# Kernel tuning notes

Measured on AMD Instinct MI355X. Metric: run time of the kernel, lower is better.

Reference implementation:

```python
import jax, jax.numpy as jnp
import numpy as np
from jax import lax

B, C, H, W = 4, 256, 64, 64
R1, R2 = 4, 8


def conv1x1(x, w, b):
    # x: [B,C,H,W], w: [O,C], b: [O]
    return jnp.einsum('bchw,oc->bohw', x, w) + b[None, :, None, None]


def dwconv3x3(x, w, b):
    # depthwise 3x3, SAME padding. w: [C,1,3,3]
    y = lax.conv_general_dilated(x, w, window_strides=(1, 1), padding='SAME',
                                 dimension_numbers=('NCHW', 'OIHW', 'NCHW'),
                                 feature_group_count=x.shape[1])
    return y + b[None, :, None, None]


def setup_inputs() -> dict:
    key = jax.random.key(0)
    ks = jax.random.split(key, 20)
    s = 0.02
    inp = {
        'x':   jax.random.normal(ks[0], (B, C, H, W), jnp.float32),
        'Wq':  jax.random.normal(ks[1], (C, C), jnp.float32) * s,
        'bq':  jnp.zeros((C,), jnp.float32),
        'Wk':  jax.random.normal(ks[2], (C, 1, 3, 3), jnp.float32) * s,
        'bk':  jnp.zeros((C,), jnp.float32),
        'Wv':  jax.random.normal(ks[3], (C, 1, 3, 3), jnp.float32) * s,
        'bv':  jnp.zeros((C,), jnp.float32),
        'Wl':  jax.random.normal(ks[4], (C, 1, 3, 3), jnp.float32) * s,
        'bl':  jnp.zeros((C,), jnp.float32),
        'Ws1': jax.random.normal(ks[5], (C // R1, C), jnp.float32) * s,
        'bs1': jnp.zeros((C // R1,), jnp.float32),
        'Ws2': jax.random.normal(ks[6], (C, C // R1), jnp.float32) * s,
        'bs2': jnp.zeros((C,), jnp.float32),
        'Wc1': jax.random.normal(ks[7], (C // R2, C), jnp.float32) * s,
        'bc1': jnp.zeros((C // R2,), jnp.float32),
        'Wc2': jax.random.normal(ks[8], (C, C // R2), jnp.float32) * s,
        'bc2': jnp.zeros((C,), jnp.float32),
        'Wo':  jax.random.normal(ks[9], (C, C), jnp.float32) * s,
        'bo':  jnp.zeros((C,), jnp.float32),
    }
    return inp


def reference(x, Wq, bq, Wk, bk, Wv, bv, Wl, bl, Ws1, bs1, Ws2, bs2,
              Wc1, bc1, Wc2, bc2, Wo, bo):
    b_, c_, h_, w_ = x.shape
    hw = h_ * w_
    scale = jnp.sqrt(jnp.float32(c_))

    q = conv1x1(x, Wq, bq).reshape(b_, c_, hw).transpose(0, 2, 1)   # [B,HW,C]
    k = dwconv3x3(x, Wk, bk).reshape(b_, c_, hw)                    # [B,C,HW]
    v_img = dwconv3x3(x, Wv, bv)                                    # [B,C,H,W]
    v = v_img.reshape(b_, c_, hw).transpose(0, 2, 1)                # [B,HW,C]

    attn = jax.nn.softmax(jnp.einsum('bnc,bcm->bnm', q, k) / scale, axis=-1)
    global_out = jnp.einsum('bnm,bmc->bnc', attn, v)                # [B,HW,C]
    global_out = global_out.transpose(0, 2, 1).reshape(b_, c_, h_, w_)

    local_out = dwconv3x3(v_img, Wl, bl)                            # [B,C,H,W]

    spatial_weight = jax.nn.sigmoid(
        conv1x1(jax.nn.relu(conv1x1(local_out, Ws1, bs1)), Ws2, bs2))

    gap = jnp.mean(global_out, axis=(2, 3), keepdims=True)          # [B,C,1,1]
    channel_weight = jax.nn.sigmoid(
        conv1x1(jax.nn.relu(conv1x1(gap, Wc1, bc1)), Wc2, bc2))     # [B,C,1,1]

    fused = global_out * channel_weight + local_out * spatial_weight
    return conv1x1(fused, Wo, bo) + x
```

## Files before the change

### kernel.cpp

```cpp
#include <hip/hip_runtime.h>
#include <hip/hip_fp8.h>
#include <stdint.h>

typedef unsigned short u16;
typedef unsigned char u8;
typedef __attribute__((ext_vector_type(8))) __bf16 bf16x8;
typedef __attribute__((ext_vector_type(8))) short short8s;
typedef __attribute__((ext_vector_type(4))) float float4v;
typedef __attribute__((ext_vector_type(16))) float floatx16;
typedef __attribute__((ext_vector_type(4))) int int4v;
typedef __attribute__((ext_vector_type(8))) int int8v;

static constexpr int NB = 4, NC = 256, NH = 64, NW = 64, NHW = 4096;
static constexpr int BC = 64;
static constexpr int NKV = 4;
static constexpr int KVCHUNK = NHW / NKV;

static constexpr size_t MB = 1ull << 20;
static constexpr size_t OFF_KBF    = 0;
static constexpr size_t OFF_LBF    = 8 * MB;
static constexpr size_t OFF_GT     = 0;
static constexpr size_t OFF_XT     = 16 * MB;
static constexpr size_t OFF_LPART  = 16 * MB;
static constexpr size_t OFF_QT8    = 24 * MB;
static constexpr size_t OFF_KT8    = 32 * MB;
static constexpr size_t OFF_V8     = 40 * MB;
static constexpr size_t OFF_LT     = 48 * MB;
static constexpr size_t OFF_OPART  = 56 * MB;
static constexpr size_t OFF_HIDT   = 88 * MB;
static constexpr size_t OFF_GAP    = OFF_HIDT + 2 * MB;
static constexpr size_t OFF_WQB    = OFF_GAP + 8 * 1024;
static constexpr size_t OFF_WS1B   = OFF_WQB + 131072;
static constexpr size_t OFF_WS2B   = OFF_WS1B + 32768;
static constexpr size_t OFF_WOB    = OFF_WS2B + 32768;

__device__ __forceinline__ float b2f(u16 h) {
    union { float f; unsigned u; } v; v.u = ((unsigned)h) << 16; return v.f;
}
__device__ __forceinline__ u16 f2b(float f) {
    union { float f; unsigned u; } v; v.f = f;
    unsigned r = v.u + 0x7fffu + ((v.u >> 16) & 1u);
    return (u16)(r >> 16);
}
__device__ __forceinline__ u8 f2f8(float f) {
    __hip_fp8_e4m3 h(f);
    return *reinterpret_cast<u8*>(&h);
}

__device__ __forceinline__ void load_lds16(const void* gsrc, void* ldst) {
    __builtin_amdgcn_global_load_lds(
        (__attribute__((address_space(1))) void*)(uintptr_t)gsrc,
        (__attribute__((address_space(3))) void*)ldst,
        16, 0, 0);
}

__global__ __launch_bounds__(256) void prep(
    const float* __restrict__ x,
    const float* __restrict__ Wq, const float* __restrict__ Ws1,
    const float* __restrict__ Ws2, const float* __restrict__ Wo,
    const float* __restrict__ Wk, const float* __restrict__ bk,
    const float* __restrict__ Wv, const float* __restrict__ bv,
    const float* __restrict__ Wl, const float* __restrict__ bl,
    u16* __restrict__ Wqb, u16* __restrict__ Ws1b, u16* __restrict__ Ws2b, u16* __restrict__ Wob,
    float* __restrict__ gap,
    u16* __restrict__ k_bf, u8* __restrict__ vN8, u16* __restrict__ local_bf,
    u16* __restrict__ xT)
{
    __shared__ __align__(16) unsigned char pshm[9216];
    const int bid = blockIdx.x;
    const int t = threadIdx.x;

    if (bid < 644) {
        int id = bid * 256 + t;
        if (id < 65536)        Wqb[id] = f2b(Wq[id]);
        else if (id < 81920)   Ws1b[id - 65536] = f2b(Ws1[id - 65536]);
        else if (id < 98304)   Ws2b[id - 81920] = f2b(Ws2[id - 81920]);
        else if (id < 163840)  Wob[id - 98304] = f2b(Wo[id - 98304]);
        else if (id < 164864)  gap[id - 163840] = 0.f;
        return;
    }
    if (bid < 2692) {
        int l = bid - 644;
        int xx0 = t & 63, cl = t >> 6;
        int y0 = (l & 7) * 8;
        int c  = ((l >> 3) & 63) * 4 + cl;
        int b  = l >> 9;
        const float* xb = x + ((size_t)b * NC + c) * NHW;
        float wk[9], wv[9], wl[9];
#pragma unroll
        for (int i = 0; i < 9; i++) { wk[i] = Wk[c*9+i]; wv[i] = Wv[c*9+i]; wl[i] = Wl[c*9+i]; }
        float bkc = bk[c], bvc = bv[c], blc = bl[c];

        auto ldx = [&](int y) -> float {
            return ((unsigned)y <= 63u) ? xb[y * 64 + xx0] : 0.f;
        };
        auto conv3 = [&](const float* w9, float a, float bm, float cc) -> float {
            float au = __shfl_up(a, 1, 64),   ad = __shfl_down(a, 1, 64);
            float bu = __shfl_up(bm, 1, 64),  bd = __shfl_down(bm, 1, 64);
            float cu = __shfl_up(cc, 1, 64),  cd = __shfl_down(cc, 1, 64);
            float al = (xx0 == 0) ? 0.f : au, ar = (xx0 == 63) ? 0.f : ad;
            float bl_ = (xx0 == 0) ? 0.f : bu, br = (xx0 == 63) ? 0.f : bd;
            float cle = (xx0 == 0) ? 0.f : cu, cr = (xx0 == 63) ? 0.f : cd;
            return w9[0]*al + w9[1]*a  + w9[2]*ar
                 + w9[3]*bl_ + w9[4]*bm + w9[5]*br
                 + w9[6]*cle + w9[7]*cc + w9[8]*cr;
        };

        float xm2 = ldx(y0 - 2), xm1 = ldx(y0 - 1), x0v = ldx(y0), xp1 = ldx(y0 + 1);
        float vm1 = (y0 - 1 >= 0) ? (bvc + conv3(wv, xm2, xm1, x0v)) : 0.f;
        float v0  = bvc + conv3(wv, xm1, x0v, xp1);

        size_t base = ((size_t)b * NC + c) * NHW;
#pragma unroll
        for (int yi = 0; yi < 8; yi++) {
            int y = y0 + yi;
            float xp2 = ldx(y + 2);
            float vp1 = (y + 1 <= 63) ? (bvc + conv3(wv, x0v, xp1, xp2)) : 0.f;
            float kk  = bkc + conv3(wk, xm1, x0v, xp1);
            float ll  = blc + conv3(wl, vm1, v0, vp1);
            size_t o = base + y * 64 + xx0;
            k_bf[o]     = f2b(kk);
            vN8[o]      = f2f8(v0);
            local_bf[o] = f2b(ll);
            xm1 = x0v; x0v = xp1; xp1 = xp2;
            vm1 = v0;  v0 = vp1;
        }
        return;
    }
    {
        u16 (*tile)[72] = reinterpret_cast<u16 (*)[72]>(pshm);
        int l = bid - 2692;
        int n0 = (l & 63) * 64;
        int c0 = ((l >> 6) & 3) * 64;
        int b  = l >> 8;
        const float* src = x + (size_t)b * NC * NHW;
        u16* dst = xT + (size_t)b * NHW * NC;
        int c = t >> 2, nb = (t & 3) * 16;
#pragma unroll
        for (int q = 0; q < 4; q++) {
            float4 v = *(const float4*)(src + (size_t)(c0 + c) * NHW + n0 + nb + q * 4);
            tile[c][nb + q * 4 + 0] = f2b(v.x);
            tile[c][nb + q * 4 + 1] = f2b(v.y);
            tile[c][nb + q * 4 + 2] = f2b(v.z);
            tile[c][nb + q * 4 + 3] = f2b(v.w);
        }
        __syncthreads();
        int cl = t & 63, ng = t >> 6;
#pragma unroll
        for (int j = 0; j < 16; j++) {
            int n = ng * 16 + j;
            dst[(size_t)(n0 + n) * NC + c0 + cl] = tile[cl][n];
        }
    }
}

__global__ __launch_bounds__(256) void mid(
    const u16* __restrict__ k_bf, const u16* __restrict__ local_bf,
    u8* __restrict__ kT8, u16* __restrict__ localT,
    const u16* __restrict__ xT, const u16* __restrict__ Wqb, const float* __restrict__ bq,
    u8* __restrict__ qT8)
{
    __shared__ __align__(16) u16 tile[64][72];
    const int t = threadIdx.x;
    const int bid = blockIdx.x;
    if (bid < 2048) {
        int n0 = (bid & 63) * 64, c0 = ((bid >> 6) & 3) * 64;
        int zb = bid >> 8, b = zb >> 1;
        const u16* src = (zb & 1) ? local_bf : k_bf;
        src += (size_t)b * NC * NHW;
        int c = t >> 2, nb = (t & 3) * 16;
        *(short8s*)&tile[c][nb]     = *(const short8s*)(src + (size_t)(c0 + c) * NHW + n0 + nb);
        *(short8s*)&tile[c][nb + 8] = *(const short8s*)(src + (size_t)(c0 + c) * NHW + n0 + nb + 8);
        __syncthreads();
        int cl = t & 63, ng = t >> 6;
        if (zb & 1) {
            u16* dst = localT + (size_t)b * NHW * NC;
#pragma unroll
            for (int j = 0; j < 16; j++) {
                int n = ng * 16 + j;
                dst[(size_t)(n0 + n) * NC + c0 + cl] = tile[cl][n];
            }
        } else {
            u8* dst = kT8 + (size_t)b * NHW * NC;
#pragma unroll
            for (int j = 0; j < 16; j++) {
                int n = ng * 16 + j;
                dst[(size_t)(n0 + n) * NC + c0 + cl] = f2f8(b2f(tile[cl][n]));
            }
        }
        return;
    }
    {
        const int w = t >> 6, lane = t & 63;
        const int lm = lane & 15, quad = lane >> 4;
        const int l = bid - 2048;
        const int b = l >> 7;
        const int s_base = (l & 127) * 32 + (w & 1) * 16;
        const int ch = (w >> 1) * 128;
        const u16* xTb = xT + (size_t)b * NHW * NC;
        u8* qTb = qT8 + (size_t)b * NHW * NC;
        bf16x8 aq[8];
#pragma unroll
        for (int kt = 0; kt < 8; kt++)
            aq[kt] = *(const bf16x8*)(xTb + (size_t)(s_base + lm) * NC + kt * 32 + quad * 8);
        float4v acc[8];
#pragma unroll
        for (int j = 0; j < 8; j++) acc[j] = (float4v){0.f, 0.f, 0.f, 0.f};
#pragma unroll
        for (int kt = 0; kt < 8; kt++) {
#pragma unroll
            for (int j = 0; j < 8; j++) {
                bf16x8 bw = *(const bf16x8*)(Wqb + (size_t)(ch + j * 16 + lm) * 256 + kt * 32 + quad * 8);
                acc[j] = __builtin_amdgcn_mfma_f32_16x16x32_bf16(aq[kt], bw, acc[j], 0, 0, 0);
            }
        }
#pragma unroll
        for (int j = 0; j < 8; j++) {
            int cout = ch + j * 16 + lm;
            float bb = bq[cout];
#pragma unroll
            for (int r = 0; r < 4; r++) {
                int s = s_base + quad * 4 + r;
                qTb[(size_t)s * NC + cout] = f2f8(acc[j][r] + bb);
            }
        }
    }
}

__device__ __forceinline__ void stage_tiles(
    const u8* __restrict__ kb, const u8* __restrict__ vb8, int kv0,
    u8* KlB, u8* VlB, int w, int lane)
{
#pragma unroll
    for (int i = 0; i < 4; i++) {
        int g = (w * 4 + i) * 64 + lane;
        int n = g >> 4, jj = g & 15, cc = jj ^ (n & 15);
        load_lds16(kb + (size_t)(kv0 + n) * NC + cc * 16, KlB + (w * 4 + i) * 1024);
    }
#pragma unroll
    for (int i = 0; i < 4; i++) {
        int g = (w * 4 + i) * 64 + lane;
        int c = g >> 2, hh = g & 3;
        int sc = hh ^ ((c >> 1) & 3);
        load_lds16(vb8 + (size_t)c * NHW + kv0 + sc * 16, VlB + (w * 4 + i) * 1024);
    }
}

__global__ __launch_bounds__(256, 2) void attn_hid(
    const u8* __restrict__ qT8, const u8* __restrict__ kT8,
    const u8* __restrict__ vN8, u8* __restrict__ Opart8, float* __restrict__ lpart,
    const u16* __restrict__ localT, const u16* __restrict__ Ws1b, const float* __restrict__ bs1,
    u16* __restrict__ hidT)
{
    __shared__ __align__(16) u8 Kl[2][BC * 256];
    __shared__ __align__(16) u8 Vl[2][256 * BC];

    const int t = threadIdx.x;
    const int w = t >> 6, lane = t & 63;

    if (blockIdx.x >= 512) {
        const int lm = lane & 15, quad = lane >> 4;
        const int l = blockIdx.x - 512;
        const int b = l >> 7;
        const int s_base = (l & 127) * 32 + (w & 1) * 16;
        const int ch = (w >> 1) * 32;
        const u16* lTb = localT + (size_t)b * NHW * NC;
        u16* hTb = hidT + (size_t)b * NHW * 64;
        bf16x8 ah[8];
#pragma unroll
        for (int kt = 0; kt < 8; kt++)
            ah[kt] = *(const bf16x8*)(lTb + (size_t)(s_base + lm) * NC + kt * 32 + quad * 8);
        float4v acc[2];
#pragma unroll
        for (int j = 0; j < 2; j++) acc[j] = (float4v){0.f, 0.f, 0.f, 0.f};
#pragma unroll
        for (int kt = 0; kt < 8; kt++) {
#pragma unroll
            for (int j = 0; j < 2; j++) {
                bf16x8 bw = *(const bf16x8*)(Ws1b + (size_t)(ch + j * 16 + lm) * 256 + kt * 32 + quad * 8);
                acc[j] = __builtin_amdgcn_mfma_f32_16x16x32_bf16(ah[kt], bw, acc[j], 0, 0, 0);
            }
        }
#pragma unroll
        for (int j = 0; j < 2; j++) {
            int h = ch + j * 16 + lm;
            float bb = bs1[h];
#pragma unroll
            for (int r = 0; r < 4; r++) {
                int s = s_base + quad * 4 + r;
                hTb[(size_t)s * 64 + h] = f2b(fmaxf(acc[j][r] + bb, 0.0f));
            }
        }
        return;
    }

    const int combo = blockIdx.x & 15;
    const int b  = combo >> 2;
    const int jc = combo & 3;
    const int n0 = (blockIdx.x >> 4) * 128;
    const int lr = lane & 31, l5 = lane >> 5;
    const int m4 = lr & 15;
    const int scl = (int)0x7F7F7F7F;

    const u8* qb = qT8 + (size_t)b * NHW * NC;
    const u8* kb = kT8 + (size_t)b * NHW * NC;
    const u8* vb8 = vN8 + (size_t)b * NC * NHW;

    int8v aqm[4];
    {
        int qrow = n0 + w * 32 + lr;
#pragma unroll
        for (int ks = 0; ks < 4; ks++)
            aqm[ks] = *(const int8v*)(qb + (size_t)qrow * NC + ks * 64 + l5 * 32);
    }

    floatx16 oacc[8];
#pragma unroll
    for (int i = 0; i < 8; i++)
#pragma unroll
        for (int j = 0; j < 16; j++) oacc[i][j] = 0.f;
    float lsum = 0.f;

    const int kvbeg = jc * KVCHUNK;
    stage_tiles(kb, vb8, kvbeg, Kl[0], Vl[0], w, lane);

    int buf = 0;
#pragma unroll 1
    for (int it = 0; it < KVCHUNK / BC; it++) {
        const int nxt = (it + 1 < KVCHUNK / BC) ? (kvbeg + (it + 1) * BC) : kvbeg;
        stage_tiles(kb, vb8, nxt, Kl[buf ^ 1], Vl[buf ^ 1], w, lane);
        asm volatile("s_waitcnt vmcnt(8)" ::: "memory");
        __builtin_amdgcn_s_barrier();

        const u8* KlB = Kl[buf];
        const u8* VlB = Vl[buf];

        unsigned uA0, uA1, uA2, uA3, uB0, uB1, uB2, uB3;

        {
            floatx16 sacc;
#pragma unroll
            for (int j = 0; j < 16; j++) sacc[j] = 0.f;
            __builtin_amdgcn_s_setprio(1);
#pragma unroll
            for (int ks = 0; ks < 4; ks++) {
                int e = ks * 4 + l5 * 2;
                int4v klo = *(const int4v*)&KlB[lr * 256 + ((e ^ m4) * 16)];
                int4v khi = *(const int4v*)&KlB[lr * 256 + (((e + 1) ^ m4) * 16)];
                int8v ka = __builtin_shufflevector(klo, khi, 0, 1, 2, 3, 4, 5, 6, 7);
                sacc = __builtin_amdgcn_mfma_scale_f32_32x32x64_f8f6f4(
                    ka, aqm[ks], sacc, 0, 0, 0, scl, 0, scl);
            }
            __builtin_amdgcn_s_setprio(0);
            float p[16];
#pragma unroll
            for (int r = 0; r < 16; r++)
                p[r] = __expf(sacc[r] * 0.0625f);
            float s0 = (p[0] + p[1]) + (p[2] + p[3]);
            float s1 = (p[4] + p[5]) + (p[6] + p[7]);
            float s2 = (p[8] + p[9]) + (p[10] + p[11]);
            float s3 = (p[12] + p[13]) + (p[14] + p[15]);
            lsum += (s0 + s1) + (s2 + s3);
            uA0 = __builtin_amdgcn_cvt_pk_fp8_f32(p[0], p[1], 0, false);
            uA0 = __builtin_amdgcn_cvt_pk_fp8_f32(p[2], p[3], uA0, true);
            uA1 = __builtin_amdgcn_cvt_pk_fp8_f32(p[4], p[5], 0, false);
            uA1 = __builtin_amdgcn_cvt_pk_fp8_f32(p[6], p[7], uA1, true);
            uA2 = __builtin_amdgcn_cvt_pk_fp8_f32(p[8], p[9], 0, false);
            uA2 = __builtin_amdgcn_cvt_pk_fp8_f32(p[10], p[11], uA2, true);
            uA3 = __builtin_amdgcn_cvt_pk_fp8_f32(p[12], p[13], 0, false);
            uA3 = __builtin_amdgcn_cvt_pk_fp8_f32(p[14], p[15], uA3, true);
        }
        {
            floatx16 sacc;
#pragma unroll
            for (int j = 0; j < 16; j++) sacc[j] = 0.f;
            __builtin_amdgcn_s_setprio(1);
#pragma unroll
            for (int ks = 0; ks < 4; ks++) {
                int e = ks * 4 + l5 * 2;
                int4v klo = *(const int4v*)&KlB[(32 + lr) * 256 + ((e ^ m4) * 16)];
                int4v khi = *(const int4v*)&KlB[(32 + lr) * 256 + (((e + 1) ^ m4) * 16)];
                int8v ka = __builtin_shufflevector(klo, khi, 0, 1, 2, 3, 4, 5, 6, 7);
                sacc = __builtin_amdgcn_mfma_scale_f32_32x32x64_f8f6f4(
                    ka, aqm[ks], sacc, 0, 0, 0, scl, 0, scl);
            }
            __builtin_amdgcn_s_setprio(0);
            float p[16];
#pragma unroll
            for (int r = 0; r < 16; r++)
                p[r] = __expf(sacc[r] * 0.0625f);
            float s0 = (p[0] + p[1]) + (p[2] + p[3]);
            float s1 = (p[4] + p[5]) + (p[6] + p[7]);
            float s2 = (p[8] + p[9]) + (p[10] + p[11]);
            float s3 = (p[12] + p[13]) + (p[14] + p[15]);
            lsum += (s0 + s1) + (s2 + s3);
            uB0 = __builtin_amdgcn_cvt_pk_fp8_f32(p[0], p[1], 0, false);
            uB0 = __builtin_amdgcn_cvt_pk_fp8_f32(p[2], p[3], uB0, true);
            uB1 = __builtin_amdgcn_cvt_pk_fp8_f32(p[4], p[5], 0, false);
            uB1 = __builtin_amdgcn_cvt_pk_fp8_f32(p[6], p[7], uB1, true);
            uB2 = __builtin_amdgcn_cvt_pk_fp8_f32(p[8], p[9], 0, false);
            uB2 = __builtin_amdgcn_cvt_pk_fp8_f32(p[10], p[11], uB2, true);
            uB3 = __builtin_amdgcn_cvt_pk_fp8_f32(p[12], p[13], 0, false);
            uB3 = __builtin_amdgcn_cvt_pk_fp8_f32(p[14], p[15], uB3, true);
        }
        asm volatile("v_permlane32_swap_b32 %0, %1" : "+v"(uA0), "+v"(uB0));
        asm volatile("v_permlane32_swap_b32 %0, %1" : "+v"(uA1), "+v"(uB1));
        asm volatile("v_permlane32_swap_b32 %0, %1" : "+v"(uA2), "+v"(uB2));
        asm volatile("v_permlane32_swap_b32 %0, %1" : "+v"(uA3), "+v"(uB3));
        int8v pa = {(int)uA0, (int)uB0, (int)uA1, (int)uB1,
                    (int)uA2, (int)uB2, (int)uA3, (int)uB3};

        __builtin_amdgcn_s_setprio(1);
#pragma unroll
        for (int ct = 0; ct < 8; ct++) {
            int c = ct * 32 + lr;
            int sw = (c >> 1) & 3;
            int4v v0 = *(const int4v*)&VlB[c * 64 + (((l5 * 2) ^ sw) * 16)];
            int4v v1 = *(const int4v*)&VlB[c * 64 + (((l5 * 2 + 1) ^ sw) * 16)];
            int8v bv = __builtin_shufflevector(v0, v1, 0, 1, 2, 3, 4, 5, 6, 7);
            oacc[ct] = __builtin_amdgcn_mfma_scale_f32_32x32x64_f8f6f4(
                pa, bv, oacc[ct], 0, 0, 0, scl, 0, scl);
        }
        __builtin_amdgcn_s_setprio(0);
        __builtin_amdgcn_s_barrier();
        buf ^= 1;
    }

    lsum += __shfl_xor(lsum, 32, 64);
    u8* Ob = Opart8 + ((size_t)(b * NKV + jc) * NHW + n0 + w * 32) * NC;
#pragma unroll
    for (int reg = 0; reg < 16; reg++) {
        int row = (reg & 3) + 8 * (reg >> 2) + 4 * l5;
#pragma unroll
        for (int ct = 0; ct < 8; ct++)
            Ob[(size_t)row * NC + ct * 32 + lr] = f2f8(oacc[ct][reg]);
    }
    if (lane < 32)
        lpart[(size_t)(b * NKV + jc) * NHW + n0 + w * 32 + lr] = lsum;
}

__global__ __launch_bounds__(256) void attn_combine(
    const u8* __restrict__ Opart8, const float* __restrict__ lpart,
    u16* __restrict__ gT, float* __restrict__ gap)
{
    __shared__ float gsum[256];
    int t = threadIdx.x;
    gsum[t] = 0.f;
    __syncthreads();
    int b = blockIdx.y;
    int n = blockIdx.x * 8 + (t >> 5);
    int c0 = (t & 31) * 8;
    float acc[8] = {};
    float l = 0.f;
#pragma unroll
    for (int j = 0; j < NKV; j++) {
        const u8* op = Opart8 + ((size_t)(b * NKV + j) * NHW + n) * NC + c0;
        unsigned long long v = *(const unsigned long long*)op;
        unsigned lo = (unsigned)v, hi = (unsigned)(v >> 32);
        acc[0] += __builtin_amdgcn_cvt_f32_fp8(lo, 0);
        acc[1] += __builtin_amdgcn_cvt_f32_fp8(lo, 1);
        acc[2] += __builtin_amdgcn_cvt_f32_fp8(lo, 2);
        acc[3] += __builtin_amdgcn_cvt_f32_fp8(lo, 3);
        acc[4] += __builtin_amdgcn_cvt_f32_fp8(hi, 0);
        acc[5] += __builtin_amdgcn_cvt_f32_fp8(hi, 1);
        acc[6] += __builtin_amdgcn_cvt_f32_fp8(hi, 2);
        acc[7] += __builtin_amdgcn_cvt_f32_fp8(hi, 3);
        l += lpart[(size_t)(b * NKV + j) * NHW + n];
    }
    float inv = 1.0f / l;
#pragma unroll
    for (int i = 0; i < 8; i++) acc[i] *= inv;
    short8s vo;
#pragma unroll
    for (int i = 0; i < 8; i++) ((u16*)&vo)[i] = f2b(acc[i]);
    *(short8s*)(gT + ((size_t)b * NHW + n) * NC + c0) = vo;
#pragma unroll
    for (int i = 0; i < 8; i++) atomicAdd(&gsum[c0 + i], acc[i]);
    __syncthreads();
    atomicAdd(&gap[b * NC + t], gsum[t]);
}

__global__ __launch_bounds__(256) void gemm_tail(
    const u16* __restrict__ hidT, const u16* __restrict__ Ws2b, const float* __restrict__ bs2,
    const u16* __restrict__ gT, const u16* __restrict__ localT,
    const float* __restrict__ gap,
    const float* __restrict__ Wc1, const float* __restrict__ bc1,
    const float* __restrict__ Wc2, const float* __restrict__ bc2,
    const u16* __restrict__ Wob, const float* __restrict__ bo,
    const float* __restrict__ x, float* __restrict__ out)
{
    __shared__ float g[256], h1[32], cwl[256];
    __shared__ float ph[32][9];
    __shared__ __align__(16) u16 fsh[32][264];
    const int t = threadIdx.x, w = t >> 6, lane = t & 63;
    const int lm = lane & 15, quad = lane >> 4;
    const int b = blockIdx.y;

    g[t] = gap[b * 256 + t] * (1.0f / 4096.0f);
    __syncthreads();
    {
        int h = t & 31, part = t >> 5;
        float s = 0.f;
        for (int c = part * 32; c < part * 32 + 32; c++) s += Wc1[h * 256 + c] * g[c];
        ph[h][part] = s;
    }
    __syncthreads();
    if (t < 32) {
        float s = bc1[t];
#pragma unroll
        for (int p = 0; p < 8; p++) s += ph[t][p];
        h1[t] = fmaxf(s, 0.f);
    }
    __syncthreads();
    {
        float s = bc2[t];
#pragma unroll
        for (int j = 0; j < 32; j++) s += Wc2[t * 32 + j] * h1[j];
        cwl[t] = 1.0f / (1.0f + __expf(-s));
    }
    __syncthreads();

    const int s_base = blockIdx.x * 32 + (w & 1) * 16;
    const int ch = (w >> 1) * 128;
    const u16* hTb = hidT + (size_t)b * NHW * 64;
    const u16* lTb = localT + (size_t)b * NHW * NC;
    const u16* gTb = gT + (size_t)b * NHW * NC;

    {
        bf16x8 ah[2];
#pragma unroll
        for (int kt = 0; kt < 2; kt++)
            ah[kt] = *(const bf16x8*)(hTb + (size_t)(s_base + lm) * 64 + kt * 32 + quad * 8);

        float4v acc[8];
#pragma unroll
        for (int j = 0; j < 8; j++) acc[j] = (float4v){0.f, 0.f, 0.f, 0.f};

#pragma unroll
        for (int kt = 0; kt < 2; kt++) {
#pragma unroll
            for (int j = 0; j < 8; j++) {
                bf16x8 bw = *(const bf16x8*)(Ws2b + (size_t)(ch + j * 16 + lm) * 64 + kt * 32 + quad * 8);
                acc[j] = __builtin_amdgcn_mfma_f32_16x16x32_bf16(ah[kt], bw, acc[j], 0, 0, 0);
            }
        }
#pragma unroll
        for (int j = 0; j < 8; j++) {
            int c = ch + j * 16 + lm;
            float bb = bs2[c];
            float cwv = cwl[c];
#pragma unroll
            for (int r = 0; r < 4; r++) {
                int s = s_base + quad * 4 + r;
                int srow = (w & 1) * 16 + quad * 4 + r;
                float sw = 1.0f / (1.0f + __expf(-(acc[j][r] + bb)));
                float gg = b2f(gTb[(size_t)s * NC + c]);
                float lo = b2f(lTb[(size_t)s * NC + c]);
                fsh[srow][c] = f2b(gg * cwv + lo * sw);
            }
        }
    }
    __syncthreads();

    {
        const int n_glob = blockIdx.x * 32;
        const int o_base = w * 64;
        float4v acc[4][2];
#pragma unroll
        for (int oj = 0; oj < 4; oj++)
#pragma unroll
            for (int nj = 0; nj < 2; nj++) acc[oj][nj] = (float4v){0.f, 0.f, 0.f, 0.f};

#pragma unroll
        for (int kt = 0; kt < 8; kt++) {
#pragma unroll
            for (int oj = 0; oj < 4; oj++) {
                bf16x8 aw = *(const bf16x8*)(Wob + (size_t)(o_base + oj * 16 + lm) * 256 + kt * 32 + quad * 8);
#pragma unroll
                for (int nj = 0; nj < 2; nj++) {
                    bf16x8 bf = *(const bf16x8*)&fsh[nj * 16 + lm][kt * 32 + quad * 8];
                    acc[oj][nj] = __builtin_amdgcn_mfma_f32_16x16x32_bf16(aw, bf, acc[oj][nj], 0, 0, 0);
                }
            }
        }
#pragma unroll
        for (int oj = 0; oj < 4; oj++) {
#pragma unroll
            for (int r = 0; r < 4; r++) {
                int o = o_base + oj * 16 + quad * 4 + r;
                float bb = bo[o];
                size_t rowoff = ((size_t)b * NC + o) * NHW;
#pragma unroll
                for (int nj = 0; nj < 2; nj++) {
                    int n = n_glob + nj * 16 + lm;
                    out[rowoff + n] = acc[oj][nj][r] + bb + x[rowoff + n];
                }
            }
        }
    }
}

extern "C" void kernel_launch(void* const* d_in, const int* in_sizes, int n_in,
                              void* d_out, int out_size, void* d_ws, size_t ws_size,
                              hipStream_t stream)
{
    const float* x   = (const float*)d_in[0];
    const float* Wq  = (const float*)d_in[1];
    const float* bq  = (const float*)d_in[2];
    const float* Wk  = (const float*)d_in[3];
    const float* bk  = (const float*)d_in[4];
    const float* Wv  = (const float*)d_in[5];
    const float* bv  = (const float*)d_in[6];
    const float* Wl  = (const float*)d_in[7];
    const float* bl  = (const float*)d_in[8];
    const float* Ws1 = (const float*)d_in[9];
    const float* bs1 = (const float*)d_in[10];
    const float* Ws2 = (const float*)d_in[11];
    const float* bs2 = (const float*)d_in[12];
    const float* Wc1 = (const float*)d_in[13];
    const float* bc1 = (const float*)d_in[14];
    const float* Wc2 = (const float*)d_in[15];
    const float* bc2 = (const float*)d_in[16];
    const float* Wo  = (const float*)d_in[17];
    const float* bo  = (const float*)d_in[18];
    float* out = (float*)d_out;

    char* ws = (char*)d_ws;
    u16* k_bf     = (u16*)(ws + OFF_KBF);
    u16* local_bf = (u16*)(ws + OFF_LBF);
    u16* gT       = (u16*)(ws + OFF_GT);
    u16* xT       = (u16*)(ws + OFF_XT);
    u8*  qT8      = (u8*)(ws + OFF_QT8);
    u8*  kT8      = (u8*)(ws + OFF_KT8);
    u8*  vN8      = (u8*)(ws + OFF_V8);
    u16* localT   = (u16*)(ws + OFF_LT);
    u8*  Opart8   = (u8*)(ws + OFF_OPART);
    float* lpart  = (float*)(ws + OFF_LPART);
    u16* hidT     = (u16*)(ws + OFF_HIDT);
    float* gap    = (float*)(ws + OFF_GAP);
    u16* Wqb      = (u16*)(ws + OFF_WQB);
    u16* Ws1b     = (u16*)(ws + OFF_WS1B);
    u16* Ws2b     = (u16*)(ws + OFF_WS2B);
    u16* Wob      = (u16*)(ws + OFF_WOB);

    prep<<<dim3(3716), 256, 0, stream>>>(x, Wq, Ws1, Ws2, Wo, Wk, bk, Wv, bv, Wl, bl,
                                         Wqb, Ws1b, Ws2b, Wob, gap, k_bf, vN8, local_bf, xT);
    mid<<<dim3(2560), 256, 0, stream>>>(k_bf, local_bf, kT8, localT, xT, Wqb, bq, qT8);
    attn_hid<<<dim3(1024), 256, 0, stream>>>(qT8, kT8, vN8, Opart8, lpart,
                                             localT, Ws1b, bs1, hidT);
    attn_combine<<<dim3(NHW / 8, 4), 256, 0, stream>>>(Opart8, lpart, gT, gap);
    gemm_tail<<<dim3(128, 4), 256, 0, stream>>>(hidT, Ws2b, bs2, gT, localT,
                                                gap, Wc1, bc1, Wc2, bc2,
                                                Wob, bo, x, out);
}
```

Measured before the change: 247.7 us.

## Fuse attention combine into tail GEMM via cooperative grid sync

Folds the attn_combine kernel into the tail kernel, which is now launched cooperatively. Each block reduces the fp8 partial outputs for its own 32 rows into shared memory and accumulates the global average pool, then a grid-wide sync waits for the pool before the channel-gate step. This drops one kernel launch and the bf16 global-output round trip through HBM, but adds a grid barrier and requires all 512 blocks to be co-resident. Separately, the softmax exponent switches from __expf to exp2f with a prescaled constant.

```diff
diff --git a/kernel.cpp b/kernel.cpp
--- a/kernel.cpp
+++ b/kernel.cpp
@@ -1,6 +1,9 @@
 #include <hip/hip_runtime.h>
 #include <hip/hip_fp8.h>
+#include <hip/hip_cooperative_groups.h>
 #include <stdint.h>
+
+namespace cg = cooperative_groups;
 
 typedef unsigned short u16;
 typedef unsigned char u8;
@@ -19,7 +22,6 @@
 static constexpr size_t MB = 1ull << 20;
 static constexpr size_t OFF_KBF    = 0;
 static constexpr size_t OFF_LBF    = 8 * MB;
-static constexpr size_t OFF_GT     = 0;
 static constexpr size_t OFF_XT     = 16 * MB;
 static constexpr size_t OFF_LPART  = 16 * MB;
 static constexpr size_t OFF_QT8    = 24 * MB;
@@ -301,6 +303,7 @@
     const int lr = lane & 31, l5 = lane >> 5;
     const int m4 = lr & 15;
     const int scl = (int)0x7F7F7F7F;
+    const float EC = 0.0901684400f;
 
     const u8* qb = qT8 + (size_t)b * NHW * NC;
     const u8* kb = kT8 + (size_t)b * NHW * NC;
@@ -355,7 +358,7 @@
             float p[16];
 #pragma unroll
             for (int r = 0; r < 16; r++)
-                p[r] = __expf(sacc[r] * 0.0625f);
+                p[r] = exp2f(sacc[r] * EC);
             float s0 = (p[0] + p[1]) + (p[2] + p[3]);
             float s1 = (p[4] + p[5]) + (p[6] + p[7]);
             float s2 = (p[8] + p[9]) + (p[10] + p[11]);
@@ -388,7 +391,7 @@
             float p[16];
 #pragma unroll
             for (int r = 0; r < 16; r++)
-                p[r] = __expf(sacc[r] * 0.0625f);
+                p[r] = exp2f(sacc[r] * EC);
             float s0 = (p[0] + p[1]) + (p[2] + p[3]);
             float s1 = (p[4] + p[5]) + (p[6] + p[7]);
             float s2 = (p[8] + p[9]) + (p[10] + p[11]);
@@ -439,51 +442,10 @@
         lpart[(size_t)(b * NKV + jc) * NHW + n0 + w * 32 + lr] = lsum;
 }
 
-__global__ __launch_bounds__(256) void attn_combine(
+__global__ __launch_bounds__(256, 2) void gemm_tail2(
+    const u16* __restrict__ hidT, const u16* __restrict__ Ws2b, const float* __restrict__ bs2,
     const u8* __restrict__ Opart8, const float* __restrict__ lpart,
-    u16* __restrict__ gT, float* __restrict__ gap)
-{
-    __shared__ float gsum[256];
-    int t = threadIdx.x;
-    gsum[t] = 0.f;
-    __syncthreads();
-    int b = blockIdx.y;
-    int n = blockIdx.x * 8 + (t >> 5);
-    int c0 = (t & 31) * 8;
-    float acc[8] = {};
-    float l = 0.f;
-#pragma unroll
-    for (int j = 0; j < NKV; j++) {
-        const u8* op = Opart8 + ((size_t)(b * NKV + j) * NHW + n) * NC + c0;
-        unsigned long long v = *(const unsigned long long*)op;
-        unsigned lo = (unsigned)v, hi = (unsigned)(v >> 32);
-        acc[0] += __builtin_amdgcn_cvt_f32_fp8(lo, 0);
-        acc[1] += __builtin_amdgcn_cvt_f32_fp8(lo, 1);
-        acc[2] += __builtin_amdgcn_cvt_f32_fp8(lo, 2);
-        acc[3] += __builtin_amdgcn_cvt_f32_fp8(lo, 3);
-        acc[4] += __builtin_amdgcn_cvt_f32_fp8(hi, 0);
-        acc[5] += __builtin_amdgcn_cvt_f32_fp8(hi, 1);
-        acc[6] += __builtin_amdgcn_cvt_f32_fp8(hi, 2);
-        acc[7] += __builtin_amdgcn_cvt_f32_fp8(hi, 3);
-        l += lpart[(size_t)(b * NKV + j) * NHW + n];
-    }
-    float inv = 1.0f / l;
-#pragma unroll
-    for (int i = 0; i < 8; i++) acc[i] *= inv;
-    short8s vo;
-#pragma unroll
-    for (int i = 0; i < 8; i++) ((u16*)&vo)[i] = f2b(acc[i]);
-    *(short8s*)(gT + ((size_t)b * NHW + n) * NC + c0) = vo;
-#pragma unroll
-    for (int i = 0; i < 8; i++) atomicAdd(&gsum[c0 + i], acc[i]);
-    __syncthreads();
-    atomicAdd(&gap[b * NC + t], gsum[t]);
-}
-
-__global__ __launch_bounds__(256) void gemm_tail(
-    const u16* __restrict__ hidT, const u16* __restrict__ Ws2b, const float* __restrict__ bs2,
-    const u16* __restrict__ gT, const u16* __restrict__ localT,
-    const float* __restrict__ gap,
+    const u16* __restrict__ localT, float* __restrict__ gap,
     const float* __restrict__ Wc1, const float* __restrict__ bc1,
     const float* __restrict__ Wc2, const float* __restrict__ bc2,
     const u16* __restrict__ Wob, const float* __restrict__ bo,
@@ -491,10 +453,52 @@
 {
     __shared__ float g[256], h1[32], cwl[256];
     __shared__ float ph[32][9];
+    __shared__ float gsum[256];
+    __shared__ __align__(16) u16 gsl[32][264];
     __shared__ __align__(16) u16 fsh[32][264];
     const int t = threadIdx.x, w = t >> 6, lane = t & 63;
     const int lm = lane & 15, quad = lane >> 4;
     const int b = blockIdx.y;
+    const int n_base0 = blockIdx.x * 32;
+
+    gsum[t] = 0.f;
+    __syncthreads();
+    {
+        int rr = t >> 5;
+        int c0 = (t & 31) * 8;
+#pragma unroll 1
+        for (int itr = 0; itr < 4; itr++) {
+            int n = n_base0 + itr * 8 + rr;
+            float acc[8] = {};
+            float l = 0.f;
+#pragma unroll
+            for (int j = 0; j < NKV; j++) {
+                const u8* op = Opart8 + ((size_t)(b * NKV + j) * NHW + n) * NC + c0;
+                unsigned long long v = *(const unsigned long long*)op;
+                unsigned lo = (unsigned)v, hi = (unsigned)(v >> 32);
+                acc[0] += __builtin_amdgcn_cvt_f32_fp8(lo, 0);
+                acc[1] += __builtin_amdgcn_cvt_f32_fp8(lo, 1);
+                acc[2] += __builtin_amdgcn_cvt_f32_fp8(lo, 2);
+                acc[3] += __builtin_amdgcn_cvt_f32_fp8(lo, 3);
+                acc[4] += __builtin_amdgcn_cvt_f32_fp8(hi, 0);
+                acc[5] += __builtin_amdgcn_cvt_f32_fp8(hi, 1);
+                acc[6] += __builtin_amdgcn_cvt_f32_fp8(hi, 2);
+                acc[7] += __builtin_amdgcn_cvt_f32_fp8(hi, 3);
+                l += lpart[(size_t)(b * NKV + j) * NHW + n];
+            }
+            float inv = 1.0f / l;
+#pragma unroll
+            for (int i = 0; i < 8; i++) acc[i] *= inv;
+#pragma unroll
+            for (int i = 0; i < 8; i++) gsl[itr * 8 + rr][c0 + i] = f2b(acc[i]);
+#pragma unroll
+            for (int i = 0; i < 8; i++) atomicAdd(&gsum[c0 + i], acc[i]);
+        }
+    }
+    __syncthreads();
+    atomicAdd(&gap[b * NC + t], gsum[t]);
+
+    cg::this_grid().sync();
 
     g[t] = gap[b * 256 + t] * (1.0f / 4096.0f);
     __syncthreads();
@@ -524,7 +528,6 @@
     const int ch = (w >> 1) * 128;
     const u16* hTb = hidT + (size_t)b * NHW * 64;
     const u16* lTb = localT + (size_t)b * NHW * NC;
-    const u16* gTb = gT + (size_t)b * NHW * NC;
 
     {
         bf16x8 ah[2];
@@ -554,7 +557,7 @@
                 int s = s_base + quad * 4 + r;
                 int srow = (w & 1) * 16 + quad * 4 + r;
                 float sw = 1.0f / (1.0f + __expf(-(acc[j][r] + bb)));
-                float gg = b2f(gTb[(size_t)s * NC + c]);
+                float gg = b2f(gsl[srow][c]);
                 float lo = b2f(lTb[(size_t)s * NC + c]);
                 fsh[srow][c] = f2b(gg * cwv + lo * sw);
             }
@@ -628,7 +631,6 @@
     char* ws = (char*)d_ws;
     u16* k_bf     = (u16*)(ws + OFF_KBF);
     u16* local_bf = (u16*)(ws + OFF_LBF);
-    u16* gT       = (u16*)(ws + OFF_GT);
     u16* xT       = (u16*)(ws + OFF_XT);
     u8*  qT8      = (u8*)(ws + OFF_QT8);
     u8*  kT8      = (u8*)(ws + OFF_KT8);
@@ -648,8 +650,12 @@
     mid<<<dim3(2560), 256, 0, stream>>>(k_bf, local_bf, kT8, localT, xT, Wqb, bq, qT8);
     attn_hid<<<dim3(1024), 256, 0, stream>>>(qT8, kT8, vN8, Opart8, lpart,
                                              localT, Ws1b, bs1, hidT);
-    attn_combine<<<dim3(NHW / 8, 4), 256, 0, stream>>>(Opart8, lpart, gT, gap);
-    gemm_tail<<<dim3(128, 4), 256, 0, stream>>>(hidT, Ws2b, bs2, gT, localT,
-                                                gap, Wc1, bc1, Wc2, bc2,
-                                                Wob, bo, x, out);
-}
+    {
+        void* args[] = {(void*)&hidT, (void*)&Ws2b, (void*)&bs2, (void*)&Opart8,
+                        (void*)&lpart, (void*)&localT, (void*)&gap,
+                        (void*)&Wc1, (void*)&bc1, (void*)&Wc2, (void*)&bc2,
+                        (void*)&Wob, (void*)&bo, (void*)&x, (void*)&out};
+        hipLaunchCooperativeKernel((void*)gemm_tail2, dim3(128, 4), dim3(256),
+                                   args, 0, stream);
+    }
+}
```

After: 305.5 us. 1.23x slower.
